# Kernel optimization log

Hardware: AMD Instinct MI355X
Metric: run time of the kernel (lower is better)

The kernel has to match this reference:

```python
import jax, jax.numpy as jnp
import numpy as np

D_MODEL = 2048
N_HEADS = 16
HEAD_DIM = D_MODEL // N_HEADS
B, T = 2, 2048


def setup_inputs() -> dict:
    key = jax.random.key(0)
    ks = jax.random.split(key, 7)
    s = 0.02
    return {
        "x": jax.random.normal(ks[0], (B, T, D_MODEL), dtype=jnp.float32),
        "w_qkv": jax.random.normal(ks[1], (D_MODEL, 3 * D_MODEL), dtype=jnp.float32) * s,
        "w_proj": jax.random.normal(ks[2], (D_MODEL, D_MODEL), dtype=jnp.float32) * s,
        "w_ff1": jax.random.normal(ks[3], (D_MODEL, 4 * D_MODEL), dtype=jnp.float32) * s,
        "b_ff1": jnp.zeros((4 * D_MODEL,), dtype=jnp.float32),
        "w_ff2": jax.random.normal(ks[4], (4 * D_MODEL, D_MODEL), dtype=jnp.float32) * s,
        "b_ff2": jnp.zeros((D_MODEL,), dtype=jnp.float32),
    }


def reference(x, w_qkv, w_proj, w_ff1, b_ff1, w_ff2, b_ff2):
    Bs, Ts, C = x.shape
    H, hd = N_HEADS, HEAD_DIM
    # fused qkv projection
    qkv = jnp.einsum("btc,cd->btd", x, w_qkv)
    q, k, v = jnp.split(qkv, 3, axis=-1)
    # (B, T, C) -> (B, H, T, hd)
    q = q.reshape(Bs, Ts, H, hd).transpose(0, 2, 1, 3)
    k = k.reshape(Bs, Ts, H, hd).transpose(0, 2, 1, 3)
    v = v.reshape(Bs, Ts, H, hd).transpose(0, 2, 1, 3)
    # paged KV write + gather round-trip (empty cache, n_kv_head == n_heads)
    # is the identity on k, v; attention is causal SDPA over the full cache.
    scale = 1.0 / jnp.sqrt(jnp.asarray(hd, dtype=x.dtype))
    scores = jnp.einsum("bhqd,bhkd->bhqk", q, k) * scale
    causal = jnp.tril(jnp.ones((Ts, Ts), dtype=bool))
    scores = jnp.where(causal, scores, jnp.finfo(scores.dtype).min)
    attn = jax.nn.softmax(scores, axis=-1)
    out = jnp.einsum("bhqk,bhkd->bhqd", attn, v)  # (B, H, T, hd)
    out = out.transpose(0, 2, 1, 3).reshape(Bs, Ts, C)
    attn_out = jnp.einsum("btc,cd->btd", out, w_proj)
    # feed-forward with exact GELU (torch nn.GELU default)
    h = jax.nn.gelu(jnp.einsum("btc,cf->btf", x, w_ff1) + b_ff1, approximate=False)
    ff_out = jnp.einsum("btf,fc->btc", h, w_ff2) + b_ff2
    return x + attn_out + ff_out
```

## Files before the change

kernel.cpp:

```cpp
#include <hip/hip_runtime.h>
#include <hip/hip_bf16.h>
#include <cmath>

typedef __bf16 bf16x8 __attribute__((ext_vector_type(8)));
typedef float f32x4 __attribute__((ext_vector_type(4)));
typedef float f32x16 __attribute__((ext_vector_type(16)));
typedef unsigned short u16;
typedef unsigned int u32;

#define DEV __device__ __forceinline__

static constexpr int BB = 2;
static constexpr int T = 2048;
static constexpr int DM = 2048;
static constexpr int NH = 16;
static constexpr int HD = 128;
static constexpr int FF = 8192;
static constexpr int M = BB * T;
static constexpr int NQKV = 3 * DM;

DEV u16 f2b(float f) {
  u32 u = __builtin_bit_cast(u32, f);
  u = (u + 0x7FFFu + ((u >> 16) & 1u)) >> 16;
  return (u16)u;
}
DEV float b2f(u16 h) {
  u32 u = ((u32)h) << 16;
  return __builtin_bit_cast(float, u);
}

DEV void gload16(const u16* g, const u16* l) {
  __builtin_amdgcn_global_load_lds(
      (const __attribute__((address_space(1))) void*)(uintptr_t)g,
      (__attribute__((address_space(3))) void*)(unsigned)(uintptr_t)l,
      16, 0, 0);
}


__global__ void cvt_f32_to_bf16(const float* __restrict__ in, u16* __restrict__ out, int n4) {
  int i = blockIdx.x * blockDim.x + threadIdx.x;
  if (i >= n4) return;
  float4 v = reinterpret_cast<const float4*>(in)[i];
  ushort4 o;
  o.x = f2b(v.x); o.y = f2b(v.y); o.z = f2b(v.z); o.w = f2b(v.w);
  reinterpret_cast<ushort4*>(out)[i] = o;
}

__global__ void transpose_cvt(const float* __restrict__ W, u16* __restrict__ Wt, int K, int N) {
  __shared__ float tile[32][33];
  int nb = blockIdx.x * 32, kb = blockIdx.y * 32;
  int r = threadIdx.x >> 3;
  int c4 = (threadIdx.x & 7) * 4;
  float4 v = *reinterpret_cast<const float4*>(&W[(size_t)(kb + r) * N + nb + c4]);
  tile[r][c4] = v.x; tile[r][c4 + 1] = v.y; tile[r][c4 + 2] = v.z; tile[r][c4 + 3] = v.w;
  __syncthreads();
  ushort4 o;
  o.x = f2b(tile[c4][r]);     o.y = f2b(tile[c4 + 1][r]);
  o.z = f2b(tile[c4 + 2][r]); o.w = f2b(tile[c4 + 3][r]);
  *reinterpret_cast<ushort4*>(&Wt[(size_t)(nb + r) * K + kb + c4]) = o;
}

__global__ void ff2_reduce(const float* __restrict__ p0, const float* __restrict__ p1,
                           const float* __restrict__ bias, const float* __restrict__ x,
                           const u16* __restrict__ ap, float* __restrict__ out) {
  int i = blockIdx.x * blockDim.x + threadIdx.x;
  float4 a = reinterpret_cast<const float4*>(p0)[i];
  float4 b = reinterpret_cast<const float4*>(p1)[i];
  float4 xx = reinterpret_cast<const float4*>(x)[i];
  float4 bi = reinterpret_cast<const float4*>(bias)[i & (DM / 4 - 1)];
  ushort4 a4 = reinterpret_cast<const ushort4*>(ap)[i];
  float4 o;
  o.x = a.x + b.x + bi.x + xx.x + b2f(a4.x);
  o.y = a.y + b.y + bi.y + xx.y + b2f(a4.y);
  o.z = a.z + b.z + bi.z + xx.z + b2f(a4.z);
  o.w = a.w + b.w + bi.w + xx.w + b2f(a4.w);
  reinterpret_cast<float4*>(out)[i] = o;
}

template <int EPI>
__global__ __launch_bounds__(512, 2) void gemm8(
    const u16* __restrict__ A, const u16* __restrict__ Bt, int Ndim,
    int Kstride, int Klen, int gx, int tpp,
    u16* __restrict__ out_bf, float* __restrict__ p0, float* __restrict__ p1,
    const float* __restrict__ bias) {
  __shared__ __align__(16) u16 lds[2 * 32768];
  const int t = threadIdx.x;
  const int nwg = gridDim.x, cpx = nwg >> 3;
  const int wg = (blockIdx.x & 7) * cpx + (blockIdx.x >> 3);
  const int part = wg / tpp, tid = wg % tpp;
  const int m0 = (tid / gx) * 256, n0 = (tid % gx) * 256;
  const int wave = t >> 6, lane = t & 63;
  const int wm = wave >> 2, wn = wave & 3;
  const int lr = lane & 15, lk = lane >> 4;

  const int srow = t >> 3;
  const int sc8 = ((t & 7) ^ (srow & 7)) * 8;
  const u16* gA = &A[(size_t)(m0 + srow) * Kstride + (size_t)part * Klen + sc8];
  const u16* gB = &Bt[(size_t)(n0 + srow) * Kstride + (size_t)part * Klen + sc8];
  const int wls = wave * 512;

  u16* buf0 = lds;
  u16* buf1 = lds + 32768;

#define STAGE_A(buf, h, kt)                                                      \
  {                                                                              \
    gload16(gA + (size_t)((h) * 128) * Kstride + (kt) * 64,                      \
            (buf) + (h) * 8192 + wls);                                           \
    gload16(gA + (size_t)((h) * 128 + 64) * Kstride + (kt) * 64,                 \
            (buf) + (h) * 8192 + 4096 + wls);                                    \
  }
#define STAGE_B(buf, h, kt)                                                      \
  {                                                                              \
    gload16(gB + (size_t)((h) * 128) * Kstride + (kt) * 64,                      \
            (buf) + 16384 + (h) * 8192 + wls);                                   \
    gload16(gB + (size_t)((h) * 128 + 64) * Kstride + (kt) * 64,                 \
            (buf) + 16384 + (h) * 8192 + 4096 + wls);                            \
  }
#define BARR                            \
  __builtin_amdgcn_sched_barrier(0);    \
  __builtin_amdgcn_s_barrier();         \
  __builtin_amdgcn_sched_barrier(0);

  const int NT = Klen >> 6;

  STAGE_B(buf0, 0, 0); STAGE_B(buf0, 1, 0);
  STAGE_A(buf0, 0, 0); STAGE_A(buf0, 1, 0);
  STAGE_B(buf1, 0, 1); STAGE_B(buf1, 1, 1);
  STAGE_A(buf1, 0, 1); STAGE_A(buf1, 1, 1);
  __builtin_amdgcn_sched_barrier(0);
  asm volatile("s_waitcnt vmcnt(8)" ::: "memory");
  __builtin_amdgcn_s_barrier();
  __builtin_amdgcn_sched_barrier(0);

  f32x4 acc[8][4] = {};
  const int aBase = (wm * 128 + lr) * 64;
  const int bBase = 16384 + (wn * 64 + lr) * 64;
  const int c0 = (lk ^ (lr & 7)) * 8;
  const int c1 = ((4 + lk) ^ (lr & 7)) * 8;

  u16* cur = buf0;
  u16* alt = buf1;
  bf16x8 a03[4][2], a47[4][2], b01[2][2], b23[2][2];

#pragma unroll
  for (int i = 0; i < 4; ++i) {
    a03[i][0] = *(const bf16x8*)&cur[aBase + i * 1024 + c0];
    a03[i][1] = *(const bf16x8*)&cur[aBase + i * 1024 + c1];
  }
#pragma unroll
  for (int j = 0; j < 2; ++j) {
    b01[j][0] = *(const bf16x8*)&cur[bBase + j * 1024 + c0];
    b01[j][1] = *(const bf16x8*)&cur[bBase + j * 1024 + c1];
  }

  for (int kt = 0; kt < NT; ++kt) {
#pragma unroll
    for (int j = 0; j < 2; ++j) {
      b23[j][0] = *(const bf16x8*)&cur[bBase + (2 + j) * 1024 + c0];
      b23[j][1] = *(const bf16x8*)&cur[bBase + (2 + j) * 1024 + c1];
    }
    __builtin_amdgcn_s_setprio(1);
#pragma unroll
    for (int i = 0; i < 4; ++i)
#pragma unroll
      for (int j = 0; j < 2; ++j)
#pragma unroll
        for (int kk = 0; kk < 2; ++kk)
          acc[i][j] = __builtin_amdgcn_mfma_f32_16x16x32_bf16(a03[i][kk], b01[j][kk], acc[i][j], 0, 0, 0);
    __builtin_amdgcn_s_setprio(0);
    BARR;
    if (kt + 2 < NT) { STAGE_B(cur, 0, kt + 2); STAGE_B(cur, 1, kt + 2); }
#pragma unroll
    for (int i = 0; i < 4; ++i) {
      a47[i][0] = *(const bf16x8*)&cur[aBase + (4 + i) * 1024 + c0];
      a47[i][1] = *(const bf16x8*)&cur[aBase + (4 + i) * 1024 + c1];
    }
    __builtin_amdgcn_s_setprio(1);
#pragma unroll
    for (int i = 0; i < 4; ++i)
#pragma unroll
      for (int j = 0; j < 2; ++j)
#pragma unroll
        for (int kk = 0; kk < 2; ++kk)
          acc[i][2 + j] = __builtin_amdgcn_mfma_f32_16x16x32_bf16(a03[i][kk], b23[j][kk], acc[i][2 + j], 0, 0, 0);
    __builtin_amdgcn_s_setprio(0);
    BARR;
    if (kt + 2 < NT) { STAGE_A(cur, 0, kt + 2); STAGE_A(cur, 1, kt + 2); }
    __builtin_amdgcn_s_setprio(1);
#pragma unroll
    for (int i = 0; i < 4; ++i)
#pragma unroll
      for (int j = 0; j < 2; ++j)
#pragma unroll
        for (int kk = 0; kk < 2; ++kk)
          acc[4 + i][j] = __builtin_amdgcn_mfma_f32_16x16x32_bf16(a47[i][kk], b01[j][kk], acc[4 + i][j], 0, 0, 0);
    __builtin_amdgcn_s_setprio(0);
    __builtin_amdgcn_sched_barrier(0);
    if (kt + 2 < NT)      asm volatile("s_waitcnt vmcnt(8)" ::: "memory");
    else if (kt + 1 < NT) asm volatile("s_waitcnt vmcnt(0)" ::: "memory");
    __builtin_amdgcn_s_barrier();
    __builtin_amdgcn_sched_barrier(0);
    if (kt + 1 < NT) {
#pragma unroll
      for (int i = 0; i < 4; ++i) {
        a03[i][0] = *(const bf16x8*)&alt[aBase + i * 1024 + c0];
        a03[i][1] = *(const bf16x8*)&alt[aBase + i * 1024 + c1];
      }
#pragma unroll
      for (int j = 0; j < 2; ++j) {
        b01[j][0] = *(const bf16x8*)&alt[bBase + j * 1024 + c0];
        b01[j][1] = *(const bf16x8*)&alt[bBase + j * 1024 + c1];
      }
    }
    __builtin_amdgcn_s_setprio(1);
#pragma unroll
    for (int i = 0; i < 4; ++i)
#pragma unroll
      for (int j = 0; j < 2; ++j)
#pragma unroll
        for (int kk = 0; kk < 2; ++kk)
          acc[4 + i][2 + j] = __builtin_amdgcn_mfma_f32_16x16x32_bf16(a47[i][kk], b23[j][kk], acc[4 + i][2 + j], 0, 0, 0);
    __builtin_amdgcn_s_setprio(0);
    BARR;
    u16* tmp = cur; cur = alt; alt = tmp;
  }
#undef STAGE_A
#undef STAGE_B
#undef BARR

  float* pout = (part == 0) ? p0 : p1;
#pragma unroll
  for (int i = 0; i < 8; ++i) {
#pragma unroll
    for (int j = 0; j < 4; ++j) {
#pragma unroll
      for (int r = 0; r < 4; ++r) {
        int gr = m0 + wm * 128 + i * 16 + (lane >> 4) * 4 + r;
        int gc = n0 + wn * 64 + j * 16 + (lane & 15);
        float v = acc[i][j][r];
        if constexpr (EPI == 0) {
          int part_ = gc >> 11, cc = gc & 2047;
          int head = cc >> 7, d = cc & 127;
          int b = gr >> 11, tt = gr & 2047;
          int bh = b * NH + head;
          size_t addr = (((size_t)(bh * 64 + (tt >> 5)) * 8 + (d >> 4)) * 512)
                        + ((tt & 31) + ((d >> 3) & 1) * 32) * 8 + (d & 7);
          out_bf[(size_t)part_ * M * DM + addr] = f2b(v);
        } else if constexpr (EPI == 2) {
          v += bias[gc];
          float u = v * (v * v * 0.044715f + 1.0f) * 0.7978845608028654f;
          float e = exp2f(u * 2.885390081777927f);
          float th = 1.0f - 2.0f / (e + 1.0f);
          v = 0.5f * v * (1.0f + th);
          out_bf[(size_t)gr * Ndim + gc] = f2b(v);
        } else {
          pout[(size_t)gr * Ndim + gc] = v;
        }
      }
    }
  }
}

template <int EPI>
__global__ __launch_bounds__(512, 4) void gemm_bf16(
    const u16* __restrict__ A, const u16* __restrict__ Bt, int Ndim, int K, int gx,
    u16* __restrict__ out_bf, float* __restrict__ out_f32,
    const float* __restrict__ bias,
    const float* __restrict__ resid_f32, const u16* __restrict__ resid_bf) {
  __shared__ __align__(16) u16 lds[3 * (256 + 128) * 32];
  const int t = threadIdx.x;
  const int nwg = gridDim.x, cpx = nwg >> 3;
  const int wg = (blockIdx.x & 7) * cpx + (blockIdx.x >> 3);
  const int m0 = (wg / gx) * 256, n0 = (wg % gx) * 128;
  const int wave = t >> 6, lane = t & 63;
  const int wm = wave >> 1, wn = wave & 1;
  const int lr = lane & 15, lk = lane >> 4;

  u16* cA = lds;                   u16* cB = lds + 8192;
  u16* nA = lds + 12288;           u16* nB = lds + 12288 + 8192;
  u16* sA = lds + 2 * 12288;       u16* sB = lds + 2 * 12288 + 8192;

  const int sk = ((lane & 3) ^ ((lane >> 3) & 3)) * 8;
  const u16* gA0 = &A[(size_t)(m0 + wave * 16 + (lane >> 2)) * K + sk];
  const u16* gA1 = gA0 + (size_t)128 * K;
  const u16* gB0 = &Bt[(size_t)(n0 + wave * 16 + (lane >> 2)) * K + sk];

  const int wbase = wave * 512;

  auto stage = [&](u16* dA, u16* dB) {
    gload16(gA0, dA + wbase);
    gload16(gA1, dA + 4096 + wbase);
    gload16(gB0, dB + wbase);
    gA0 += 32; gA1 += 32; gB0 += 32;
  };

  const int NT = K >> 5;

  stage(cA, cB);
  stage(nA, nB);
  __builtin_amdgcn_sched_barrier(0);
  asm volatile("s_waitcnt vmcnt(3)" ::: "memory");
  __builtin_amdgcn_s_barrier();
  __builtin_amdgcn_sched_barrier(0);

  f32x4 acc[4][4] = {};
  const int rcol = (lk ^ ((lr >> 1) & 3)) * 8;

  for (int kt = 0; kt < NT; ++kt) {
    if (kt + 2 < NT) stage(sA, sB);
    bf16x8 af[4], bfr[4];
#pragma unroll
    for (int i = 0; i < 4; ++i) {
      af[i]  = *reinterpret_cast<const bf16x8*>(&cA[(wm * 64 + i * 16 + lr) * 32 + rcol]);
      bfr[i] = *reinterpret_cast<const bf16x8*>(&cB[(wn * 64 + i * 16 + lr) * 32 + rcol]);
    }
#pragma unroll
    for (int i = 0; i < 4; ++i)
#pragma unroll
      for (int j = 0; j < 4; ++j)
        acc[i][j] = __builtin_amdgcn_mfma_f32_16x16x32_bf16(af[i], bfr[j], acc[i][j], 0, 0, 0);
    if (kt + 1 < NT) {
      __builtin_amdgcn_sched_barrier(0);
      if (kt + 2 < NT) asm volatile("s_waitcnt vmcnt(3)" ::: "memory");
      else             asm volatile("s_waitcnt vmcnt(0)" ::: "memory");
      __builtin_amdgcn_s_barrier();
      __builtin_amdgcn_sched_barrier(0);
      u16* tA = cA; u16* tB = cB;
      cA = nA; cB = nB; nA = sA; nB = sB; sA = tA; sB = tB;
    }
  }

#pragma unroll
  for (int i = 0; i < 4; ++i) {
#pragma unroll
    for (int j = 0; j < 4; ++j) {
#pragma unroll
      for (int r = 0; r < 4; ++r) {
        int gr = m0 + wm * 64 + i * 16 + (lane >> 4) * 4 + r;
        int gc = n0 + wn * 64 + j * 16 + (lane & 15);
        float v = acc[i][j][r];
        if constexpr (EPI == 1) {
          out_bf[(size_t)gr * Ndim + gc] = f2b(v);
        } else if constexpr (EPI == 3) {
          v += bias[gc] + resid_f32[(size_t)gr * Ndim + gc] + b2f(resid_bf[(size_t)gr * Ndim + gc]);
          out_f32[(size_t)gr * Ndim + gc] = v;
        } else {
          int hh = gr >> 7, d = gr & 127;
          int b = gc >> 11, tt = gc & 2047;
          int bh = b * NH + hh;
          size_t addr = (((size_t)(bh * 128 + (tt >> 4)) * 4 + (d >> 5)) * 512)
                        + ((d & 31) + ((tt >> 3) & 1) * 32) * 8 + (tt & 7);
          out_bf[addr] = f2b(v);
        }
      }
    }
  }
}

__global__ __launch_bounds__(256) void attn_frag(
    const u16* __restrict__ qf_, const u16* __restrict__ kf_,
    const u16* __restrict__ vf_, u16* __restrict__ outg) {
  const int l = threadIdx.x & 63;
  const int wq = threadIdx.x >> 6;
  const int bh = blockIdx.y;
  const int qi = gridDim.x - 1 - blockIdx.x;
  const int qb = qi * 4 + wq;
  const int h = l >> 5, ln = l & 31;
  const int qrow = qb * 32 + ln;

  const u16* qbase = qf_ + ((size_t)(bh * 64 + qb) * 8) * 512 + l * 8;
  bf16x8 qf[8];
#pragma unroll
  for (int s = 0; s < 8; ++s)
    qf[s] = *reinterpret_cast<const bf16x8*>(qbase + s * 512);

  f32x16 acc0 = {}, acc1 = {}, acc2 = {}, acc3 = {};
  float mrow = -INFINITY, lrow = 0.f;
  const float scaleL = 0.08838834764831845f * 1.4426950408889634f;
  const int ntiles = qb + 1;

  for (int kt = 0; kt < ntiles; ++kt) {
    const u16* kbase = kf_ + ((size_t)(bh * 64 + kt) * 8) * 512 + l * 8;
    f32x16 sa = {};
#pragma unroll
    for (int s = 0; s < 8; ++s) {
      bf16x8 kf = *reinterpret_cast<const bf16x8*>(kbase + s * 512);
      sa = __builtin_amdgcn_mfma_f32_32x32x16_bf16(kf, qf[s], sa, 0, 0, 0);
    }

    float p[16];
    float lmax = -INFINITY;
    const bool diag = (kt == qb);
#pragma unroll
    for (int r = 0; r < 16; ++r) {
      float sv = sa[r] * scaleL;
      if (diag) {
        int kv = kt * 32 + (r & 3) + 8 * (r >> 2) + 4 * h;
        if (kv > qrow) sv = -INFINITY;
      }
      p[r] = sv;
      lmax = fmaxf(lmax, sv);
    }
    float rmax = fmaxf(lmax, __shfl_xor(lmax, 32));

    if (__any(rmax > mrow + 11.5f)) {
      float mnew = fmaxf(mrow, rmax);
      float corr = exp2f(mrow - mnew);
      mrow = mnew;
      lrow *= corr;
#pragma unroll
      for (int r = 0; r < 16; ++r) {
        float cr = __shfl(corr, (r & 3) + 8 * (r >> 2) + 4 * h);
        acc0[r] *= cr; acc1[r] *= cr; acc2[r] *= cr; acc3[r] *= cr;
      }
    }

    float ls = 0.f;
#pragma unroll
    for (int r = 0; r < 16; ++r) {
      p[r] = exp2f(p[r] - mrow);
      ls += p[r];
    }
    lrow += ls + __shfl_xor(ls, 32);

    u32 w[8];
#pragma unroll
    for (int c = 0; c < 8; ++c)
      asm("v_cvt_pk_bf16_f32 %0, %1, %2" : "=v"(w[c]) : "v"(p[2 * c]), "v"(p[2 * c + 1]));
    u32 x[8];
#pragma unroll
    for (int c = 0; c < 8; ++c) x[c] = (u32)__shfl_xor((int)w[c], 32);
    uint4 A0, A1;
    A0.x = h ? x[2] : w[0]; A0.y = h ? x[3] : w[1];
    A0.z = h ? w[2] : x[0]; A0.w = h ? w[3] : x[1];
    A1.x = h ? x[6] : w[4]; A1.y = h ? x[7] : w[5];
    A1.z = h ? w[6] : x[4]; A1.w = h ? w[7] : x[5];
    bf16x8 pa0 = __builtin_bit_cast(bf16x8, A0);
    bf16x8 pa1 = __builtin_bit_cast(bf16x8, A1);

    const u16* vbase = vf_ + ((size_t)(bh * 128 + kt * 2) * 4) * 512 + l * 8;
    bf16x8 v0, v1;
    v0 = *reinterpret_cast<const bf16x8*>(vbase + 0 * 512);
    v1 = *reinterpret_cast<const bf16x8*>(vbase + 4 * 512);
    acc0 = __builtin_amdgcn_mfma_f32_32x32x16_bf16(pa0, v0, acc0, 0, 0, 0);
    acc0 = __builtin_amdgcn_mfma_f32_32x32x16_bf16(pa1, v1, acc0, 0, 0, 0);
    v0 = *reinterpret_cast<const bf16x8*>(vbase + 1 * 512);
    v1 = *reinterpret_cast<const bf16x8*>(vbase + 5 * 512);
    acc1 = __builtin_amdgcn_mfma_f32_32x32x16_bf16(pa0, v0, acc1, 0, 0, 0);
    acc1 = __builtin_amdgcn_mfma_f32_32x32x16_bf16(pa1, v1, acc1, 0, 0, 0);
    v0 = *reinterpret_cast<const bf16x8*>(vbase + 2 * 512);
    v1 = *reinterpret_cast<const bf16x8*>(vbase + 6 * 512);
    acc2 = __builtin_amdgcn_mfma_f32_32x32x16_bf16(pa0, v0, acc2, 0, 0, 0);
    acc2 = __builtin_amdgcn_mfma_f32_32x32x16_bf16(pa1, v1, acc2, 0, 0, 0);
    v0 = *reinterpret_cast<const bf16x8*>(vbase + 3 * 512);
    v1 = *reinterpret_cast<const bf16x8*>(vbase + 7 * 512);
    acc3 = __builtin_amdgcn_mfma_f32_32x32x16_bf16(pa0, v0, acc3, 0, 0, 0);
    acc3 = __builtin_amdgcn_mfma_f32_32x32x16_bf16(pa1, v1, acc3, 0, 0, 0);
  }

  const int b = bh >> 4, hh = bh & 15;
#pragma unroll
  for (int r = 0; r < 16; ++r) {
    int qr = (r & 3) + 8 * (r >> 2) + 4 * h;
    float lr = __shfl(lrow, qr);
    float rl = 1.0f / lr;
    int tt = qb * 32 + qr;
    size_t rowoff = ((size_t)(b * T + tt)) * DM + hh * HD + ln;
    outg[rowoff + 0]  = f2b(acc0[r] * rl);
    outg[rowoff + 32] = f2b(acc1[r] * rl);
    outg[rowoff + 64] = f2b(acc2[r] * rl);
    outg[rowoff + 96] = f2b(acc3[r] * rl);
  }
}


extern "C" void kernel_launch(void* const* d_in, const int* in_sizes, int n_in,
                              void* d_out, int out_size, void* d_ws, size_t ws_size,
                              hipStream_t stream) {
  const float* x      = (const float*)d_in[0];
  const float* w_qkv  = (const float*)d_in[1];
  const float* w_proj = (const float*)d_in[2];
  const float* w_ff1  = (const float*)d_in[3];
  const float* b_ff1  = (const float*)d_in[4];
  const float* w_ff2  = (const float*)d_in[5];
  const float* b_ff2  = (const float*)d_in[6];
  float* out = (float*)d_out;

  u16* ws = (u16*)d_ws;
  size_t o = 0;
  u16* x_bf      = ws + o; o += (size_t)M * DM;
  u16* wqkv_t    = ws + o; o += (size_t)NQKV * DM;
  u16* wproj_t   = ws + o; o += (size_t)DM * DM;
  u16* wff1_t    = ws + o; o += (size_t)FF * DM;
  u16* wff2_t    = ws + o; o += (size_t)DM * FF;
  u16* attn_proj = ws + o; o += (size_t)M * DM;
  u16* qbuf      = ws + o;
  u16* kbuf      = qbuf + (size_t)M * DM;
  u16* vtbuf     = kbuf + (size_t)M * DM;
  u16* attn_out  = vtbuf + (size_t)M * DM;
  u16* hbuf      = qbuf;

  float* p0 = (float*)ws;
  float* p1 = (float*)wff1_t;

  cvt_f32_to_bf16<<<(M * DM / 4 + 255) / 256, 256, 0, stream>>>(x, x_bf, M * DM / 4);
  transpose_cvt<<<dim3(NQKV / 32, DM / 32), 256, 0, stream>>>(w_qkv, wqkv_t, DM, NQKV);
  transpose_cvt<<<dim3(DM / 32, DM / 32), 256, 0, stream>>>(w_proj, wproj_t, DM, DM);
  transpose_cvt<<<dim3(FF / 32, DM / 32), 256, 0, stream>>>(w_ff1, wff1_t, DM, FF);
  transpose_cvt<<<dim3(DM / 32, FF / 32), 256, 0, stream>>>(w_ff2, wff2_t, FF, DM);

  gemm8<0><<<256, 512, 0, stream>>>(x_bf, wqkv_t, 4096, DM, DM, 16, 256,
                                    qbuf, nullptr, nullptr, nullptr);

  gemm_bf16<4><<<256, 512, 0, stream>>>(
      wqkv_t + (size_t)4096 * DM, x_bf, M, DM, 32, vtbuf, nullptr, nullptr, nullptr, nullptr);

  attn_frag<<<dim3(T / 128, BB * NH), 256, 0, stream>>>(qbuf, kbuf, vtbuf, attn_out);

  gemm_bf16<1><<<256, 512, 0, stream>>>(
      attn_out, wproj_t, DM, DM, 16, attn_proj, nullptr, nullptr, nullptr, nullptr);

  gemm8<2><<<512, 512, 0, stream>>>(x_bf, wff1_t, FF, DM, DM, 32, 512,
                                    hbuf, nullptr, nullptr, b_ff1);

  gemm8<5><<<256, 512, 0, stream>>>(hbuf, wff2_t, DM, FF, 4096, 8, 128,
                                    nullptr, p0, p1, nullptr);

  ff2_reduce<<<M * DM / 4 / 256, 256, 0, stream>>>(p0, p1, b_ff2, x, attn_proj, out);
}
```

Measured before the change: 625.7 us.

## Fuse V projection into QKV GEMM and launch attention with one wave per block

The QKV GEMM now covers all three parts (Q, K and V) and writes V directly in the transposed fragment layout that attention expects. This removes the separate gemm_bf16<4> launch that recomputed V^T from x. Attention blocks shrink from four waves to one wave per 32-row query block, giving more, smaller blocks that may balance the causal workload better across CUs. The trade-off is that the V stores are scattered, and the four-wave grouping that shared scheduling is lost.

New measurement: 647.0 us. 1.03x slower.

```diff
diff --git a/kernel.cpp b/kernel.cpp
--- a/kernel.cpp
+++ b/kernel.cpp
@@ -243,8 +243,13 @@
           int head = cc >> 7, d = cc & 127;
           int b = gr >> 11, tt = gr & 2047;
           int bh = b * NH + head;
-          size_t addr = (((size_t)(bh * 64 + (tt >> 5)) * 8 + (d >> 4)) * 512)
-                        + ((tt & 31) + ((d >> 3) & 1) * 32) * 8 + (d & 7);
+          size_t addr;
+          if (part_ < 2)
+            addr = (((size_t)(bh * 64 + (tt >> 5)) * 8 + (d >> 4)) * 512)
+                   + ((tt & 31) + ((d >> 3) & 1) * 32) * 8 + (d & 7);
+          else
+            addr = (((size_t)(bh * 128 + (tt >> 4)) * 4 + (d >> 5)) * 512)
+                   + ((d & 31) + ((tt >> 3) & 1) * 32) * 8 + (tt & 7);
           out_bf[(size_t)part_ * M * DM + addr] = f2b(v);
         } else if constexpr (EPI == 2) {
           v += bias[gc];
@@ -264,9 +269,7 @@
 template <int EPI>
 __global__ __launch_bounds__(512, 4) void gemm_bf16(
     const u16* __restrict__ A, const u16* __restrict__ Bt, int Ndim, int K, int gx,
-    u16* __restrict__ out_bf, float* __restrict__ out_f32,
-    const float* __restrict__ bias,
-    const float* __restrict__ resid_f32, const u16* __restrict__ resid_bf) {
+    u16* __restrict__ out_bf) {
   __shared__ __align__(16) u16 lds[3 * (256 + 128) * 32];
   const int t = threadIdx.x;
   const int nwg = gridDim.x, cpx = nwg >> 3;
@@ -338,33 +341,18 @@
       for (int r = 0; r < 4; ++r) {
         int gr = m0 + wm * 64 + i * 16 + (lane >> 4) * 4 + r;
         int gc = n0 + wn * 64 + j * 16 + (lane & 15);
-        float v = acc[i][j][r];
-        if constexpr (EPI == 1) {
-          out_bf[(size_t)gr * Ndim + gc] = f2b(v);
-        } else if constexpr (EPI == 3) {
-          v += bias[gc] + resid_f32[(size_t)gr * Ndim + gc] + b2f(resid_bf[(size_t)gr * Ndim + gc]);
-          out_f32[(size_t)gr * Ndim + gc] = v;
-        } else {
-          int hh = gr >> 7, d = gr & 127;
-          int b = gc >> 11, tt = gc & 2047;
-          int bh = b * NH + hh;
-          size_t addr = (((size_t)(bh * 128 + (tt >> 4)) * 4 + (d >> 5)) * 512)
-                        + ((d & 31) + ((tt >> 3) & 1) * 32) * 8 + (tt & 7);
-          out_bf[addr] = f2b(v);
-        }
+        out_bf[(size_t)gr * Ndim + gc] = f2b(acc[i][j][r]);
       }
     }
   }
 }
 
-__global__ __launch_bounds__(256) void attn_frag(
+__global__ __launch_bounds__(64) void attn_frag(
     const u16* __restrict__ qf_, const u16* __restrict__ kf_,
     const u16* __restrict__ vf_, u16* __restrict__ outg) {
   const int l = threadIdx.x & 63;
-  const int wq = threadIdx.x >> 6;
   const int bh = blockIdx.y;
-  const int qi = gridDim.x - 1 - blockIdx.x;
-  const int qb = qi * 4 + wq;
+  const int qb = gridDim.x - 1 - blockIdx.x;
   const int h = l >> 5, ln = l & 31;
   const int qrow = qb * 32 + ln;
 
@@ -496,8 +484,8 @@
   u16* attn_proj = ws + o; o += (size_t)M * DM;
   u16* qbuf      = ws + o;
   u16* kbuf      = qbuf + (size_t)M * DM;
-  u16* vtbuf     = kbuf + (size_t)M * DM;
-  u16* attn_out  = vtbuf + (size_t)M * DM;
+  u16* vbuf      = kbuf + (size_t)M * DM;
+  u16* attn_out  = vbuf + (size_t)M * DM;
   u16* hbuf      = qbuf;
 
   float* p0 = (float*)ws;
@@ -509,16 +497,13 @@
   transpose_cvt<<<dim3(FF / 32, DM / 32), 256, 0, stream>>>(w_ff1, wff1_t, DM, FF);
   transpose_cvt<<<dim3(DM / 32, FF / 32), 256, 0, stream>>>(w_ff2, wff2_t, FF, DM);
 
-  gemm8<0><<<256, 512, 0, stream>>>(x_bf, wqkv_t, 4096, DM, DM, 16, 256,
+  gemm8<0><<<384, 512, 0, stream>>>(x_bf, wqkv_t, NQKV, DM, DM, 24, 384,
                                     qbuf, nullptr, nullptr, nullptr);
 
-  gemm_bf16<4><<<256, 512, 0, stream>>>(
-      wqkv_t + (size_t)4096 * DM, x_bf, M, DM, 32, vtbuf, nullptr, nullptr, nullptr, nullptr);
-
-  attn_frag<<<dim3(T / 128, BB * NH), 256, 0, stream>>>(qbuf, kbuf, vtbuf, attn_out);
+  attn_frag<<<dim3(T / 32, BB * NH), 64, 0, stream>>>(qbuf, kbuf, vbuf, attn_out);
 
   gemm_bf16<1><<<256, 512, 0, stream>>>(
-      attn_out, wproj_t, DM, DM, 16, attn_proj, nullptr, nullptr, nullptr, nullptr);
+      attn_out, wproj_t, DM, DM, 16, attn_proj);
 
   gemm8<2><<<512, 512, 0, stream>>>(x_bf, wff1_t, FF, DM, DM, 32, 512,
                                     hbuf, nullptr, nullptr, b_ff1);
```
